# Kernel optimization log

Hardware: AMD Instinct MI355X
Metric: run time of the kernel (lower is better)

Reference implementation:

```python
import jax, jax.numpy as jnp
import numpy as np

N = 4096
IN_SIZE = 512
MLP_W = 16
HID = 512
MID = 64  # hardcoded tgc2 output size in the torch module
OUT = 128
BN_EPS = 1e-5


def setup_inputs() -> dict:
    key = jax.random.key(0)
    ks = jax.random.split(key, 24)
    adj = (jax.random.uniform(ks[0], (N, N)) < 0.05).astype(jnp.float32)
    xdeg = jax.random.uniform(ks[1], (N, N), dtype=jnp.float32)
    ydeg = jax.random.uniform(ks[2], (N, N), dtype=jnp.float32)
    u = lambda k, sh, fan: jax.random.uniform(k, sh, jnp.float32, -1.0, 1.0) / np.sqrt(fan)
    return {
        "adj": adj, "xdeg": xdeg, "ydeg": ydeg,
        # edge MLP: 3 -> MLP_W -> 2
        "mlp_w1": u(ks[3], (3, MLP_W), 3), "mlp_b1": jnp.zeros((MLP_W,), jnp.float32),
        "mlp_w2": u(ks[4], (MLP_W, 2), MLP_W), "mlp_b2": jnp.zeros((2,), jnp.float32),
        # positional linear: Linear(N, in_size) applied to eye(N) -> pe = W^T + b
        "pe_w": u(ks[5], (N, IN_SIZE), N), "pe_b": jnp.zeros((IN_SIZE,), jnp.float32),
        # GCN weights
        "gc1_w": u(ks[6], (IN_SIZE, HID), HID),
        "lin2_w": u(ks[7], (HID, MID), HID), "lin2_b": jnp.zeros((MID,), jnp.float32),
        "gc3_w": u(ks[8], (MID, OUT), OUT),
        # BatchNorm (eval mode: running stats)
        "bn1_g": jnp.ones((HID,), jnp.float32), "bn1_b": jnp.zeros((HID,), jnp.float32),
        "bn1_m": jnp.zeros((HID,), jnp.float32), "bn1_v": jnp.ones((HID,), jnp.float32),
        "bn2_g": jnp.ones((OUT,), jnp.float32), "bn2_b": jnp.zeros((OUT,), jnp.float32),
        "bn2_m": jnp.zeros((OUT,), jnp.float32), "bn2_v": jnp.ones((OUT,), jnp.float32),
    }


def reference(adj, xdeg, ydeg, mlp_w1, mlp_b1, mlp_w2, mlp_b2, pe_w, pe_b,
              gc1_w, lin2_w, lin2_b, gc3_w,
              bn1_g, bn1_b, bn1_m, bn1_v, bn2_g, bn2_b, bn2_m, bn2_v):
    # Edge MLP + softmax over [adj, xdeg, ydeg] features; torch only computes it
    # at nonzero adj entries then scatters into a dense mask. Since the mask is
    # multiplied by adj, computing densely and multiplying is exactly equivalent.
    feats = jnp.stack([adj, xdeg, ydeg], axis=-1)          # [N, N, 3]
    h = jax.nn.relu(jnp.einsum('nmf,fw->nmw', feats, mlp_w1) + mlp_b1)
    logits = jnp.einsum('nmw,wc->nmc', h, mlp_w2) + mlp_b2  # [N, N, 2]
    mask = jax.nn.softmax(logits, axis=-1)[..., 1]          # [N, N]
    a = adj * mask + jnp.eye(adj.shape[0], dtype=adj.dtype)

    # Degree normalization: A' = D_row^{-1/2} A D_col^{-1/2} (broadcast, no diag matmuls)
    rowsum = jnp.sum(a, axis=1)
    colsum = jnp.sum(a, axis=0)
    d_row = jnp.where(rowsum > 0, rowsum ** -0.5, 0.0)
    d_col = jnp.where(colsum > 0, colsum ** -0.5, 0.0)
    a = d_row[:, None] * a * d_col[None, :]

    # pe = Linear(eye(N)) = W^T + b (eval mode, dropout off)
    pe = pe_w + pe_b[None, :]                               # [N, IN_SIZE]

    h = a @ (pe @ gc1_w)                                    # GCN layer 1
    h = (h - bn1_m) * (bn1_g / jnp.sqrt(bn1_v + BN_EPS)) + bn1_b
    h = h @ lin2_w + lin2_b                                 # tgc2
    mid = h
    h = jax.nn.relu(h)
    h = a @ (h @ gc3_w)                                     # GCN layer 3
    out = (h - bn2_m) * (bn2_g / jnp.sqrt(bn2_v + BN_EPS)) + bn2_b
    return out, mid
```

## Files before the change

### kernel.cpp

```cpp
#include <hip/hip_runtime.h>
#include <hip/hip_bf16.h>

#define NN 4096
#define INS 512
#define HIDW 512
#define MIDW 64
#define OUTW 128
#define CAP 384
#define SEG 96
#define BN_EPS 1e-5f
#define NSTRIP 8
#define NPAIR (NSTRIP / 2)
#define SLOTCAP (NSTRIP * SEG)
#define CS_BLOCKS 512
#define CS_ROWS 8
#define K3_LDS 25600

__device__ __forceinline__ void thin_block(
    const float* __restrict__ A, const float* __restrict__ B,
    const float* __restrict__ abias, float* __restrict__ C, int K, int bb,
    float (*As)[36], float (*Bs)[64])
{
    const int t = threadIdx.x;
    const int bm = bb * 32;
    const int c2 = t & 31, rg = t >> 5;

    float acc[4][2] = {};
    for (int k0 = 0; k0 < K; k0 += 64) {
        #pragma unroll
        for (int l = 0; l < 8; ++l) {
            int e = t + l * 256;
            int r = e >> 6, k = e & 63;
            float v = A[(size_t)(bm + r) * K + k0 + k];
            if (abias) v += abias[k0 + k];
            As[k][r] = v;
        }
        #pragma unroll
        for (int l = 0; l < 16; ++l) {
            int e = t + l * 256;
            int k = e >> 6, n = e & 63;
            Bs[k][n] = B[(size_t)(k0 + k) * 64 + n];
        }
        __syncthreads();
        #pragma unroll
        for (int k = 0; k < 64; ++k) {
            float4 a4 = *reinterpret_cast<const float4*>(&As[k][rg * 4]);
            float2 b2 = *reinterpret_cast<const float2*>(&Bs[k][2 * c2]);
            acc[0][0] = fmaf(a4.x, b2.x, acc[0][0]);
            acc[0][1] = fmaf(a4.x, b2.y, acc[0][1]);
            acc[1][0] = fmaf(a4.y, b2.x, acc[1][0]);
            acc[1][1] = fmaf(a4.y, b2.y, acc[1][1]);
            acc[2][0] = fmaf(a4.z, b2.x, acc[2][0]);
            acc[2][1] = fmaf(a4.z, b2.y, acc[2][1]);
            acc[3][0] = fmaf(a4.w, b2.x, acc[3][0]);
            acc[3][1] = fmaf(a4.w, b2.y, acc[3][1]);
        }
        __syncthreads();
    }
    #pragma unroll
    for (int u = 0; u < 4; ++u) {
        int r = bm + rg * 4 + u;
        *reinterpret_cast<float2*>(&C[(size_t)r * 64 + 2 * c2]) =
            make_float2(acc[u][0], acc[u][1]);
    }
}

__global__ __launch_bounds__(256) void k_count_prep(
    const float* __restrict__ adj,
    int* __restrict__ cslot, int* __restrict__ cnt, int* __restrict__ dflag,
    const float* __restrict__ lin2_w, const float* __restrict__ lin2_b,
    const float* __restrict__ bn1_g, const float* __restrict__ bn1_b,
    const float* __restrict__ bn1_m, const float* __restrict__ bn1_v,
    const float* __restrict__ bn2_g, const float* __restrict__ bn2_b,
    const float* __restrict__ bn2_m, const float* __restrict__ bn2_v,
    float* __restrict__ Wp, float* __restrict__ c1,
    float* __restrict__ s2g, float* __restrict__ t2g)
{
    const int t = threadIdx.x;
    if (blockIdx.x == 0) {
        __shared__ float t1s[HIDW];
        for (int h = t; h < HIDW; h += 256) {
            float s1 = bn1_g[h] * rsqrtf(bn1_v[h] + BN_EPS);
            t1s[h] = bn1_b[h] - bn1_m[h] * s1;
            for (int m = 0; m < MIDW; ++m)
                Wp[(size_t)h * MIDW + m] = s1 * lin2_w[(size_t)h * MIDW + m];
        }
        __syncthreads();
        if (t < MIDW) {
            float acc = lin2_b[t];
            for (int h = 0; h < HIDW; ++h)
                acc = fmaf(t1s[h], lin2_w[(size_t)h * MIDW + t], acc);
            c1[t] = acc;
        } else if (t >= 64 && t < 64 + OUTW) {
            int j = t - 64;
            float s2 = bn2_g[j] * rsqrtf(bn2_v[j] + BN_EPS);
            s2g[j] = s2;
            t2g[j] = bn2_b[j] - bn2_m[j] * s2;
        }
        return;
    }
    const int wave = t >> 6, lane = t & 63;
    const int gw = (blockIdx.x - 1) * 4 + wave;
    const int i = gw >> 3, s = gw & 7;
    const int colbase = s * 512;
    const float* __restrict__ base = adj + (size_t)i * NN + colbase + 4 * lane;
    float4 a4a = *reinterpret_cast<const float4*>(base);
    float4 a4b = *reinterpret_cast<const float4*>(base + 256);
    const float av[8] = {a4a.x, a4a.y, a4a.z, a4a.w,
                         a4b.x, a4b.y, a4b.z, a4b.w};
    int* __restrict__ slot = cslot + (size_t)i * SLOTCAP + s * SEG;
    const unsigned long long lt = (1ULL << lane) - 1ULL;
    int run = 0;
    #pragma unroll
    for (int c = 0; c < 8; ++c) {
        int col = colbase + ((c < 4) ? (4 * lane + c) : (256 + 4 * lane + c - 4));
        bool diag = (col == i);
        bool act = (av[c] != 0.f) || diag;
        if (diag) dflag[i] = (av[c] != 0.f) ? 1 : 0;
        unsigned long long m = __ballot(act);
        if (act) {
            int pos = run + __popcll(m & lt);
            if (pos < SEG) slot[pos] = col;
        }
        run += __popcll(m);
    }
    if (lane == 0) cnt[gw] = (run < SEG) ? run : SEG;
}

__global__ __launch_bounds__(256) void k_fill_w2(
    const float* __restrict__ xdeg, const float* __restrict__ ydeg,
    const int* __restrict__ cslot, const int* __restrict__ cnt,
    const int* __restrict__ dflag,
    const float* __restrict__ w1, const float* __restrict__ b1,
    const float* __restrict__ w2, const float* __restrict__ b2,
    float* __restrict__ a_vals, int* __restrict__ a_cols,
    float* __restrict__ rs_part,
    const float* __restrict__ gc1_w, const float* __restrict__ Wp,
    float* __restrict__ W2)
{
    __shared__ float As[64][36];
    __shared__ float Bs[64][64];
    if (blockIdx.x < INS / 32) {
        thin_block(gc1_w, Wp, nullptr, W2, HIDW, blockIdx.x, As, Bs);
        return;
    }
    __shared__ float shb[16], sw1x[16], sw1y[16], sw2[32], sb2[2];
    const int t = threadIdx.x;
    const int wave = t >> 6, lane = t & 63;
    if (t < 16) {
        shb[t]  = b1[t] + w1[t];
        sw1x[t] = w1[16 + t];
        sw1y[t] = w1[32 + t];
    }
    if (t < 32) sw2[t] = w2[t];
    if (t < 2)  sb2[t] = b2[t];
    __syncthreads();

    const int q = __builtin_amdgcn_readfirstlane(
        (blockIdx.x - INS / 32) * 4 + wave);
    const int i = q >> 2;
    const int sp = (q & 3) * 2;
    const int* __restrict__ cb = cnt + i * NSTRIP;
    int wb = 0;
    #pragma unroll
    for (int ss = 0; ss < NSTRIP; ++ss) if (ss < sp) wb += cb[ss];
    const int n0 = cb[sp];
    const int ntot = n0 + cb[sp + 1];
    const int hasde = dflag[i];
    const int* __restrict__ slot = cslot + (size_t)i * SLOTCAP + sp * SEG;
    const float* __restrict__ xrow = xdeg + (size_t)i * NN;
    const float* __restrict__ yrow = ydeg + (size_t)i * NN;
    float* __restrict__ gv = a_vals + (size_t)i * CAP;
    int*   __restrict__ gc = a_cols + (size_t)i * CAP;

    float local = 0.f;
    for (int p = lane; p < ntot; p += 64) {
        int col = (p < n0) ? slot[p] : slot[SEG + p - n0];
        float x = xrow[col];
        float y = yrow[col];
        float l0 = sb2[0], l1 = sb2[1];
        #pragma unroll
        for (int w = 0; w < 16; ++w) {
            float hw = fmaf(x, sw1x[w], shb[w]);
            hw = fmaf(y, sw1y[w], hw);
            hw = fmaxf(hw, 0.f);
            l0 = fmaf(hw, sw2[2 * w],     l0);
            l1 = fmaf(hw, sw2[2 * w + 1], l1);
        }
        float v = 1.f / (1.f + __expf(l0 - l1));
        if (col == i) v = hasde ? (v + 1.f) : 1.f;
        int gp = wb + p;
        if (gp < CAP) { gc[gp] = col; gv[gp] = v; }
        local += v;
    }
    #pragma unroll
    for (int o = 32; o >= 1; o >>= 1)
        local += __shfl_down(local, o, 64);
    if (lane == 0) rs_part[q] = local;
}

__global__ __launch_bounds__(256) void k_colsum_g(
    const float* __restrict__ a_vals, const int* __restrict__ a_cols,
    const int* __restrict__ cnt, float* __restrict__ P,
    const float* __restrict__ pe_w, const float* __restrict__ pe_b,
    const float* __restrict__ W2, float* __restrict__ G)
{
    extern __shared__ char smem3[];
    if (blockIdx.x < NN / 32) {
        float (*As)[36] = reinterpret_cast<float (*)[36]>(smem3);
        float (*Bs)[64] = reinterpret_cast<float (*)[64]>(smem3 + 9216);
        thin_block(pe_w, W2, pe_b, G, INS, blockIdx.x, As, Bs);
        return;
    }
    float* ls = reinterpret_cast<float*>(smem3);
    const int t = threadIdx.x;
    const int wave = t >> 6, lane = t & 63;
    const int b = blockIdx.x - NN / 32;
    for (int j = t; j < NN; j += 256) ls[j] = 0.f;
    __syncthreads();
    const int r0 = b * CS_ROWS;
    #pragma unroll
    for (int rr = 0; rr < 2; ++rr) {
        const int r = r0 + wave * 2 + rr;
        int n = 0;
        #pragma unroll
        for (int ss = 0; ss < NSTRIP; ++ss) n += cnt[r * NSTRIP + ss];
        n = (n < CAP) ? n : CAP;
        const float* __restrict__ vr = a_vals + (size_t)r * CAP;
        const int*   __restrict__ cr = a_cols + (size_t)r * CAP;
        for (int p0 = 4 * lane; p0 < n; p0 += 256) {
            float4 v4 = *reinterpret_cast<const float4*>(vr + p0);
            int4   c4 = *reinterpret_cast<const int4*>(cr + p0);
            if (p0 + 0 < n) atomicAdd(&ls[c4.x], v4.x);
            if (p0 + 1 < n) atomicAdd(&ls[c4.y], v4.y);
            if (p0 + 2 < n) atomicAdd(&ls[c4.z], v4.z);
            if (p0 + 3 < n) atomicAdd(&ls[c4.w], v4.w);
        }
    }
    __syncthreads();
    for (int j = t; j < NN; j += 256)
        P[(size_t)b * NN + j] = ls[j];
}

__global__ __launch_bounds__(512) void k_scale(
    const float* __restrict__ rs_part, const float* __restrict__ P,
    float* __restrict__ d_row, float* __restrict__ d_col)
{
    int j = blockIdx.x * 512 + threadIdx.x;
    float r = 0.f;
    #pragma unroll
    for (int s = 0; s < NPAIR; ++s) r += rs_part[j * NPAIR + s];
    d_row[j] = (r > 0.f) ? 1.f / sqrtf(r) : 0.f;
    float c = 0.f;
    for (int b = 0; b < CS_BLOCKS; ++b)
        c += P[(size_t)b * NN + j];
    d_col[j] = (c > 0.f) ? 1.f / sqrtf(c) : 0.f;
}

template <bool WITH_MID>
__global__ __launch_bounds__(256) void k_spmm(
    const float* __restrict__ a_vals, const int* __restrict__ a_cols,
    const int* __restrict__ cnt, const float* __restrict__ X,
    const float* __restrict__ d_row, const float* __restrict__ d_col,
    const float* __restrict__ c1,
    const float* __restrict__ gc3, const float* __restrict__ s2g,
    const float* __restrict__ t2g,
    float* __restrict__ O1, float* __restrict__ O2)
{
    __shared__ float sv[2][CAP];
    __shared__ int   scl[2][CAP];
    __shared__ float sacc[4][64];
    const int t = threadIdx.x;
    const int wave = t >> 6, lane = t & 63;
    const int rb = wave >> 1, h = wave & 1;
    const int i = blockIdx.x * 2 + rb;
    int n = 0;
    #pragma unroll
    for (int ss = 0; ss < NSTRIP; ++ss) n += cnt[i * NSTRIP + ss];
    n = (n < CAP) ? n : CAP;
    const int n16 = (n + 15) & ~15;
    const float* __restrict__ vrow = a_vals + (size_t)i * CAP;
    const int*   __restrict__ crow = a_cols + (size_t)i * CAP;

    for (int p = h * 64 + lane; p < n16; p += 128) {
        bool ok = p < n;
        int c = ok ? crow[p] : 0;
        float v = ok ? vrow[p] : 0.f;
        if (WITH_MID) v *= d_col[c];
        sv[rb][p]  = v;
        scl[rb][p] = c;
    }
    __syncthreads();

    const int eh = lane >> 5;
    const int lc = lane & 31;
    const int Q  = n16 >> 1;
    const int Qh = Q >> 1;

    float a0 = 0.f, a1 = 0.f;
    for (int q = h * Qh; q < (h + 1) * Qh; q += 4) {
        #pragma unroll
        for (int j = 0; j < 4; ++j) {
            int p = 2 * (q + j) + eh;
            float v = sv[rb][p];
            int c = scl[rb][p];
            float2 x = *reinterpret_cast<const float2*>(X + (size_t)c * 64 + 2 * lc);
            a0 = fmaf(v, x.x, a0);
            a1 = fmaf(v, x.y, a1);
        }
    }
    a0 += __shfl_xor(a0, 32);
    a1 += __shfl_xor(a1, 32);
    if (lane < 32) { sacc[wave][2 * lc] = a0; sacc[wave][2 * lc + 1] = a1; }
    __syncthreads();

    if (WITH_MID) {
        if (h == 0 && lane < 32) {
            float s0 = sacc[wave][2 * lc]     + sacc[wave + 1][2 * lc];
            float s1 = sacc[wave][2 * lc + 1] + sacc[wave + 1][2 * lc + 1];
            float dr = d_row[i];
            float dc = d_col[i];
            float m0 = fmaf(s0, dr, c1[2 * lc]);
            float m1 = fmaf(s1, dr, c1[2 * lc + 1]);
            *reinterpret_cast<float2*>(O1 + (size_t)i * 64 + 2 * lc) =
                make_float2(m0, m1);
            *reinterpret_cast<float2*>(O2 + (size_t)i * 64 + 2 * lc) =
                make_float2(dc * fmaxf(m0, 0.f), dc * fmaxf(m1, 0.f));
        }
    } else {
        if (h == 0 && lane < 32) {
            float dr = d_row[i];
            float s0 = (sacc[wave][2 * lc]     + sacc[wave + 1][2 * lc])     * dr;
            float s1 = (sacc[wave][2 * lc + 1] + sacc[wave + 1][2 * lc + 1]) * dr;
            sacc[wave][2 * lc]     = s0;
            sacc[wave][2 * lc + 1] = s1;
        }
        __syncthreads();
        const int rb2 = t >> 7;
        const int j = t & 127;
        const float* __restrict__ srow = sacc[2 * rb2];
        float acc = 0.f;
        #pragma unroll 8
        for (int k = 0; k < 64; ++k)
            acc = fmaf(srow[k], gc3[k * 128 + j], acc);
        int orow = blockIdx.x * 2 + rb2;
        O1[(size_t)orow * 128 + j] = fmaf(acc, s2g[j], t2g[j]);
    }
}

extern "C" void kernel_launch(void* const* d_in, const int* in_sizes, int n_in,
                              void* d_out, int out_size, void* d_ws, size_t ws_size,
                              hipStream_t stream) {
    const float* adj    = (const float*)d_in[0];
    const float* xdeg   = (const float*)d_in[1];
    const float* ydeg   = (const float*)d_in[2];
    const float* mlp_w1 = (const float*)d_in[3];
    const float* mlp_b1 = (const float*)d_in[4];
    const float* mlp_w2 = (const float*)d_in[5];
    const float* mlp_b2 = (const float*)d_in[6];
    const float* pe_w   = (const float*)d_in[7];
    const float* pe_b   = (const float*)d_in[8];
    const float* gc1_w  = (const float*)d_in[9];
    const float* lin2_w = (const float*)d_in[10];
    const float* lin2_b = (const float*)d_in[11];
    const float* gc3_w  = (const float*)d_in[12];
    const float* bn1_g  = (const float*)d_in[13];
    const float* bn1_b  = (const float*)d_in[14];
    const float* bn1_m  = (const float*)d_in[15];
    const float* bn1_v  = (const float*)d_in[16];
    const float* bn2_g  = (const float*)d_in[17];
    const float* bn2_b  = (const float*)d_in[18];
    const float* bn2_m  = (const float*)d_in[19];
    const float* bn2_v  = (const float*)d_in[20];

    float* out = (float*)d_out;
    float* mid = out + (size_t)NN * OUTW;

    char* w = (char*)d_ws;
    float* a_vals = (float*)w;  w += (size_t)NN * CAP * 4;
    int*   a_cols = (int*)w;    w += (size_t)NN * CAP * 4;
    int*   cslot  = (int*)w;    w += (size_t)NN * SLOTCAP * 4;
    int*   cnt    = (int*)w;    w += (size_t)NN * NSTRIP * 4;
    int*   dflag  = (int*)w;    w += (size_t)NN * 4;
    float* rs_part= (float*)w;  w += (size_t)NN * NPAIR * 4;
    float* d_row  = (float*)w;  w += (size_t)NN * 4;
    float* d_col  = (float*)w;  w += (size_t)NN * 4;
    float* P      = (float*)w;  w += (size_t)CS_BLOCKS * NN * 4;
    float* Wp     = (float*)w;  w += (size_t)HIDW * MIDW * 4;
    float* W2     = (float*)w;  w += (size_t)INS * MIDW * 4;
    float* c1     = (float*)w;  w += 256;
    float* s2g    = (float*)w;  w += 512;
    float* t2g    = (float*)w;  w += 512;
    float* G      = (float*)w;  w += (size_t)NN * MIDW * 4;
    float* R      = (float*)w;  w += (size_t)NN * MIDW * 4;

    k_count_prep<<<NN * NSTRIP / 4 + 1, 256, 0, stream>>>(
        adj, cslot, cnt, dflag, lin2_w, lin2_b, bn1_g, bn1_b, bn1_m, bn1_v,
        bn2_g, bn2_b, bn2_m, bn2_v, Wp, c1, s2g, t2g);
    k_fill_w2<<<INS / 32 + NN * NPAIR / 4, 256, 0, stream>>>(
        xdeg, ydeg, cslot, cnt, dflag, mlp_w1, mlp_b1, mlp_w2, mlp_b2,
        a_vals, a_cols, rs_part, gc1_w, Wp, W2);
    k_colsum_g<<<NN / 32 + CS_BLOCKS, 256, K3_LDS, stream>>>(
        a_vals, a_cols, cnt, P, pe_w, pe_b, W2, G);
    k_scale<<<NN / 512, 512, 0, stream>>>(rs_part, P, d_row, d_col);
    k_spmm<true><<<NN / 2, 256, 0, stream>>>(
        a_vals, a_cols, cnt, G, d_row, d_col, c1,
        nullptr, nullptr, nullptr, mid, R);
    k_spmm<false><<<NN / 2, 256, 0, stream>>>(
        a_vals, a_cols, cnt, R, d_row, d_col, nullptr,
        gc3_w, s2g, t2g, out, nullptr);
}
```

Before: 141.6 us.

## Split fused colsum/thin-GEMM kernel, batch thin loads, halve colsum partial blocks

Splits the combined kernel that ran both the thin pe·W2 GEMM and the column-sum atomics into two separate launches with static LDS. The colsum blocks now each cover 16 rows, so there are half as many blocks and half as many partial rows for k_scale to reduce. The thin GEMM tile loads are first gathered into registers and then written to LDS, so global loads can overlap. The cost is one extra kernel launch, the loss of overlap between the two workloads, and fewer colsum blocks to spread across the GPU.

```diff
diff --git a/kernel.cpp b/kernel.cpp
--- a/kernel.cpp
+++ b/kernel.cpp
@@ -12,9 +12,8 @@
 #define NSTRIP 8
 #define NPAIR (NSTRIP / 2)
 #define SLOTCAP (NSTRIP * SEG)
-#define CS_BLOCKS 512
-#define CS_ROWS 8
-#define K3_LDS 25600
+#define CS_BLOCKS 256
+#define CS_ROWS 16
 
 __device__ __forceinline__ void thin_block(
     const float* __restrict__ A, const float* __restrict__ B,
@@ -27,19 +26,29 @@
 
     float acc[4][2] = {};
     for (int k0 = 0; k0 < K; k0 += 64) {
+        float va[8];
         #pragma unroll
         for (int l = 0; l < 8; ++l) {
             int e = t + l * 256;
-            int r = e >> 6, k = e & 63;
-            float v = A[(size_t)(bm + r) * K + k0 + k];
-            if (abias) v += abias[k0 + k];
-            As[k][r] = v;
-        }
+            va[l] = A[(size_t)(bm + (e >> 6)) * K + k0 + (e & 63)];
+        }
+        float vb[16];
         #pragma unroll
         for (int l = 0; l < 16; ++l) {
             int e = t + l * 256;
-            int k = e >> 6, n = e & 63;
-            Bs[k][n] = B[(size_t)(k0 + k) * 64 + n];
+            vb[l] = B[(size_t)(k0 + (e >> 6)) * 64 + (e & 63)];
+        }
+        #pragma unroll
+        for (int l = 0; l < 8; ++l) {
+            int e = t + l * 256;
+            float v = va[l];
+            if (abias) v += abias[k0 + (e & 63)];
+            As[e & 63][e >> 6] = v;
+        }
+        #pragma unroll
+        for (int l = 0; l < 16; ++l) {
+            int e = t + l * 256;
+            Bs[e >> 6][e & 63] = vb[l];
         }
         __syncthreads();
         #pragma unroll
@@ -199,29 +208,29 @@
     if (lane == 0) rs_part[q] = local;
 }
 
-__global__ __launch_bounds__(256) void k_colsum_g(
-    const float* __restrict__ a_vals, const int* __restrict__ a_cols,
-    const int* __restrict__ cnt, float* __restrict__ P,
+__global__ __launch_bounds__(256) void k_thin_g(
     const float* __restrict__ pe_w, const float* __restrict__ pe_b,
     const float* __restrict__ W2, float* __restrict__ G)
 {
-    extern __shared__ char smem3[];
-    if (blockIdx.x < NN / 32) {
-        float (*As)[36] = reinterpret_cast<float (*)[36]>(smem3);
-        float (*Bs)[64] = reinterpret_cast<float (*)[64]>(smem3 + 9216);
-        thin_block(pe_w, W2, pe_b, G, INS, blockIdx.x, As, Bs);
-        return;
-    }
-    float* ls = reinterpret_cast<float*>(smem3);
+    __shared__ float As[64][36];
+    __shared__ float Bs[64][64];
+    thin_block(pe_w, W2, pe_b, G, INS, blockIdx.x, As, Bs);
+}
+
+__global__ __launch_bounds__(256) void k_colsum(
+    const float* __restrict__ a_vals, const int* __restrict__ a_cols,
+    const int* __restrict__ cnt, float* __restrict__ P)
+{
+    __shared__ float ls[NN];
     const int t = threadIdx.x;
     const int wave = t >> 6, lane = t & 63;
-    const int b = blockIdx.x - NN / 32;
+    const int b = blockIdx.x;
     for (int j = t; j < NN; j += 256) ls[j] = 0.f;
     __syncthreads();
     const int r0 = b * CS_ROWS;
     #pragma unroll
-    for (int rr = 0; rr < 2; ++rr) {
-        const int r = r0 + wave * 2 + rr;
+    for (int rr = 0; rr < 4; ++rr) {
+        const int r = r0 + wave * 4 + rr;
         int n = 0;
         #pragma unroll
         for (int ss = 0; ss < NSTRIP; ++ss) n += cnt[r * NSTRIP + ss];
@@ -400,8 +409,8 @@
     k_fill_w2<<<INS / 32 + NN * NPAIR / 4, 256, 0, stream>>>(
         xdeg, ydeg, cslot, cnt, dflag, mlp_w1, mlp_b1, mlp_w2, mlp_b2,
         a_vals, a_cols, rs_part, gc1_w, Wp, W2);
-    k_colsum_g<<<NN / 32 + CS_BLOCKS, 256, K3_LDS, stream>>>(
-        a_vals, a_cols, cnt, P, pe_w, pe_b, W2, G);
+    k_thin_g<<<NN / 32, 256, 0, stream>>>(pe_w, pe_b, W2, G);
+    k_colsum<<<CS_BLOCKS, 256, 0, stream>>>(a_vals, a_cols, cnt, P);
     k_scale<<<NN / 512, 512, 0, stream>>>(rs_part, P, d_row, d_col);
     k_spmm<true><<<NN / 2, 256, 0, stream>>>(
         a_vals, a_cols, cnt, G, d_row, d_col, c1,
```

Measured after the change: 122.8 us. 1.15x faster.
